# Kernel tuning notes

Measured on AMD Instinct MI355X. Metric: run time of the kernel, lower is better.

## Reference

```python
import jax, jax.numpy as jnp
import numpy as np

N_NODES = 50000
N_EDGES = 800000
IN_DIM, HID_DIM, OUT_DIM = 512, 64, 40
DROPOUT_P = 0.5


def _gcn_conv(h, src, dst, deg_inv_sqrt, W, b, n_nodes):
    # PyG GCNConv (normalize=True, add_self_loops=True):
    #   h' = h @ W; out[dst] += d^-1/2[src] * d^-1/2[dst] * h'[src]; out += b
    # src/dst already include self-loops; deg_inv_sqrt precomputed from them.
    ht = h @ W                                            # [N, F_out]
    norm = deg_inv_sqrt[src] * deg_inv_sqrt[dst]          # [E+N]
    msg = ht[src] * norm[:, None]                         # [E+N, F_out]
    out = jax.ops.segment_sum(msg, dst, num_segments=n_nodes)
    return out + b


def setup_inputs() -> dict:
    key = jax.random.key(0)
    k1, k2, k3, k4 = jax.random.split(key, 4)
    x = jax.random.normal(k1, (N_NODES, IN_DIM), dtype=jnp.float32)
    edge_index = jax.random.randint(k2, (2, N_EDGES), 0, N_NODES, dtype=jnp.int32)
    W1 = jax.random.normal(k3, (IN_DIM, HID_DIM), dtype=jnp.float32) / np.sqrt(IN_DIM)
    b1 = jnp.zeros((HID_DIM,), dtype=jnp.float32)
    W2 = jax.random.normal(k4, (HID_DIM, OUT_DIM), dtype=jnp.float32) / np.sqrt(HID_DIM)
    b2 = jnp.zeros((OUT_DIM,), dtype=jnp.float32)
    return {"x": x, "edge_index": edge_index, "W1": W1, "b1": b1, "W2": W2, "b2": b2}


def reference(x, edge_index, W1, b1, W2, b2):
    n = x.shape[0]
    loop = jnp.arange(n, dtype=edge_index.dtype)
    src = jnp.concatenate([edge_index[0], loop])          # add self-loops
    dst = jnp.concatenate([edge_index[1], loop])
    deg = jax.ops.segment_sum(jnp.ones_like(dst, dtype=x.dtype), dst, num_segments=n)
    deg_inv_sqrt = jnp.where(deg > 0, jax.lax.rsqrt(deg), 0.0)

    h = _gcn_conv(x, src, dst, deg_inv_sqrt, W1, b1, n)
    h = jax.nn.relu(h)
    # dropout (training=True) with a fixed key for determinism
    keep = jax.random.bernoulli(jax.random.key(42), 1.0 - DROPOUT_P, h.shape)
    h = jnp.where(keep, h / (1.0 - DROPOUT_P), 0.0)
    h = _gcn_conv(h, src, dst, deg_inv_sqrt, W2, b2, n)
    return jax.nn.log_softmax(h, axis=1)
```

## Files before the change

kernel.cpp:

```cpp
#include <hip/hip_runtime.h>
#include <math.h>
#include <float.h>

#define N_NODES 50000
#define N_EDGES 800000
#define IN_DIM  512
#define HID_DIM 64
#define OUT_DIM 40
#define GEMM1_BLOCKS 782
#define FILL_BLOCKS 1568
#define NODES_PER_GRP 6250
#define BCAP 96
#define AGG_Q 1563
#define AGG_BLOCKS (8 * AGG_Q)

typedef __attribute__((ext_vector_type(8))) short bf16x8;
typedef __attribute__((ext_vector_type(4))) float f32x4;

__device__ __forceinline__ unsigned rotl32(unsigned v, int n) {
  return (v << n) | (v >> (32 - n));
}

__device__ __forceinline__ void threefry2x32_0_42(unsigned x0, unsigned x1,
                                                  unsigned &o0, unsigned &o1) {
  const unsigned ks0 = 0u;
  const unsigned ks1 = 42u;
  const unsigned ks2 = 0u ^ 42u ^ 0x1BD11BDAu;
  x0 += ks0; x1 += ks1;
  x0 += x1; x1 = rotl32(x1, 13); x1 ^= x0;
  x0 += x1; x1 = rotl32(x1, 15); x1 ^= x0;
  x0 += x1; x1 = rotl32(x1, 26); x1 ^= x0;
  x0 += x1; x1 = rotl32(x1,  6); x1 ^= x0;
  x0 += ks1; x1 += ks2 + 1u;
  x0 += x1; x1 = rotl32(x1, 17); x1 ^= x0;
  x0 += x1; x1 = rotl32(x1, 29); x1 ^= x0;
  x0 += x1; x1 = rotl32(x1, 16); x1 ^= x0;
  x0 += x1; x1 = rotl32(x1, 24); x1 ^= x0;
  x0 += ks2; x1 += ks0 + 2u;
  x0 += x1; x1 = rotl32(x1, 13); x1 ^= x0;
  x0 += x1; x1 = rotl32(x1, 15); x1 ^= x0;
  x0 += x1; x1 = rotl32(x1, 26); x1 ^= x0;
  x0 += x1; x1 = rotl32(x1,  6); x1 ^= x0;
  x0 += ks0; x1 += ks1 + 3u;
  x0 += x1; x1 = rotl32(x1, 17); x1 ^= x0;
  x0 += x1; x1 = rotl32(x1, 29); x1 ^= x0;
  x0 += x1; x1 = rotl32(x1, 16); x1 ^= x0;
  x0 += x1; x1 = rotl32(x1, 24); x1 ^= x0;
  x0 += ks1; x1 += ks2 + 4u;
  x0 += x1; x1 = rotl32(x1, 13); x1 ^= x0;
  x0 += x1; x1 = rotl32(x1, 15); x1 ^= x0;
  x0 += x1; x1 = rotl32(x1, 26); x1 ^= x0;
  x0 += x1; x1 = rotl32(x1,  6); x1 ^= x0;
  x0 += ks2; x1 += ks0 + 5u;
  o0 = x0; o1 = x1;
}

__device__ __forceinline__ unsigned short f2bf(float f) {
  unsigned u = __float_as_uint(f);
  unsigned r = u + 0x7FFFu + ((u >> 16) & 1u);
  return (unsigned short)(r >> 16);
}

__global__ void k_init(const float* __restrict__ W1, const float* __restrict__ W2,
                       unsigned short* __restrict__ Wb1, float* __restrict__ w2t,
                       int* __restrict__ cnt) {
  int i = blockIdx.x * 256 + threadIdx.x;
  if (i < N_NODES) cnt[i] = 0;
  if (i < IN_DIM * HID_DIM) {
    int j = i & 7;
    int lane = (i >> 3) & 63;
    int cg = (i >> 9) & 3;
    int kb = i >> 11;
    int k = kb * 32 + ((lane >> 4) << 3) + j;
    int c = cg * 16 + (lane & 15);
    Wb1[i] = f2bf(W1[k * HID_DIM + c]);
  }
  if (i < HID_DIM * OUT_DIM) {
    int j = i >> 6;
    int k = i & 63;
    w2t[i] = W2[k * OUT_DIM + j];
  }
}

#define XS 136
__global__ __launch_bounds__(512) void k_gemm1_fill(
    const int* __restrict__ ei, int* __restrict__ cnt,
    unsigned short* __restrict__ elist2,
    const float* __restrict__ x, const unsigned short* __restrict__ Wb1,
    unsigned short* __restrict__ ht1b) {
  __shared__ unsigned short sxa[2][64 * XS];

  if (blockIdx.x >= GEMM1_BLOCKS) {
    const int fb = blockIdx.x - GEMM1_BLOCKS;
    const int grp = blockIdx.x & 7;
    const int ord = fb >> 3;
    const int lo = grp * NODES_PER_GRP;
    const int hi = lo + NODES_PER_GRP;
    const int ebase = ord * 512 + threadIdx.x;
    int dv[8];
#pragma unroll
    for (int i = 0; i < 8; ++i) {
      int e = ebase + i * (196 * 512);
      dv[i] = (e < N_EDGES) ? ei[N_EDGES + e] : -1;
    }
#pragma unroll
    for (int i = 0; i < 8; ++i) {
      if (dv[i] >= lo && dv[i] < hi) {
        int s = ei[ebase + i * (196 * 512)];
        int slot = atomicAdd(&cnt[dv[i]], 1);
        if (slot < BCAP) elist2[dv[i] * BCAP + slot] = (unsigned short)s;
      }
    }
    return;
  }

  const int tid = threadIdx.x;
  const int lane = tid & 63;
  const int wave = tid >> 6;
  const int brow = blockIdx.x * 64;
  const int sr = tid >> 3;
  const int sq = tid & 7;

  f32x4 acc[2];
  acc[0] = (f32x4){0.f, 0.f, 0.f, 0.f};
  acc[1] = (f32x4){0.f, 0.f, 0.f, 0.f};

  const bf16x8* __restrict__ Wv = (const bf16x8*)Wb1;
  int gr = brow + sr;
  if (gr >= N_NODES) gr = N_NODES - 1;
  const float* __restrict__ xrow = x + (size_t)gr * IN_DIM;

  float4 lv[4];
#define LOADR(K0)                                                             \
  {                                                                           \
    _Pragma("unroll")                                                         \
    for (int j = 0; j < 4; ++j)                                               \
      lv[j] = *(const float4*)(xrow + (K0) + (sq + j * 8) * 4);               \
  }
#define WRITE(B)                                                              \
  {                                                                           \
    _Pragma("unroll")                                                         \
    for (int j = 0; j < 4; ++j) {                                             \
      ushort4 o;                                                              \
      o.x = f2bf(lv[j].x); o.y = f2bf(lv[j].y);                               \
      o.z = f2bf(lv[j].z); o.w = f2bf(lv[j].w);                               \
      *(ushort4*)(&sxa[B][sr * XS + (sq + j * 8) * 4]) = o;                   \
    }                                                                         \
  }

  LOADR(0)
  WRITE(0)
  __syncthreads();

  const int arow = (16 * (wave & 3) + (lane & 15)) * XS + ((lane >> 4) << 3);
  const int cgb = 2 * (wave >> 2);

  int buf = 0;
  for (int kc = 0; kc < 4; ++kc) {
    if (kc < 3) LOADR((kc + 1) * 128)
#pragma unroll
    for (int ks = 0; ks < 4; ++ks) {
      bf16x8 a = *(const bf16x8*)(&sxa[buf][arow + ks * 32]);
      int kb = kc * 4 + ks;
#pragma unroll
      for (int c = 0; c < 2; ++c) {
        bf16x8 b = Wv[(kb * 4 + cgb + c) * 64 + lane];
        acc[c] = __builtin_amdgcn_mfma_f32_16x16x32_bf16(a, b, acc[c], 0, 0, 0);
      }
    }
    if (kc < 3) WRITE(buf ^ 1)
    __syncthreads();
    buf ^= 1;
  }
#undef LOADR
#undef WRITE

#pragma unroll
  for (int q = 0; q < 4; ++q) {
    int grow = brow + 16 * (wave & 3) + ((lane >> 4) << 2) + q;
    if (grow < N_NODES) {
#pragma unroll
      for (int c = 0; c < 2; ++c) {
        ht1b[(size_t)grow * HID_DIM + (cgb + c) * 16 + (lane & 15)] =
            f2bf(acc[c][q]);
      }
    }
  }
}

__global__ __launch_bounds__(256) void k_agg1g2(const int* __restrict__ cnt,
                                                const unsigned short* __restrict__ elist2,
                                                const unsigned short* __restrict__ ht1b,
                                                const float* __restrict__ b1,
                                                const float* __restrict__ w2t,
                                                unsigned short* __restrict__ ht2b) {
  const int wave = threadIdx.x >> 6;
  const int lane = threadIdx.x & 63;
  const int dl = (blockIdx.x >> 3) * 4 + wave;
  if (dl >= NODES_PER_GRP) return;
  const int d = (blockIdx.x & 7) * NODES_PER_GRP + dl;
  const int g = lane >> 3;
  const int fh = lane & 7;

  unsigned t0, t1;
  threefry2x32_0_42(0u, (unsigned)d * 64u + (unsigned)lane, t0, t1);
  unsigned long long keep = __ballot(!((t0 ^ t1) & 0x80000000u));

  int cn = cnt[d];
  if (cn > BCAP) cn = BCAP;
  const unsigned short* __restrict__ bucket = elist2 + d * BCAP;
  float4 a0 = {0.f, 0.f, 0.f, 0.f};
  float4 a1 = {0.f, 0.f, 0.f, 0.f};
#pragma unroll 2
  for (int j = g; j < cn; j += 8) {
    int s = bucket[j];
    float ds = rsqrtf((float)cnt[s] + 1.0f);
    const uint2* __restrict__ p = (const uint2*)(ht1b + (size_t)s * HID_DIM);
    uint2 q0 = p[fh];
    uint2 q1 = p[fh + 8];
    a0.x += __uint_as_float(q0.x << 16) * ds;
    a0.y += __uint_as_float(q0.x & 0xFFFF0000u) * ds;
    a0.z += __uint_as_float(q0.y << 16) * ds;
    a0.w += __uint_as_float(q0.y & 0xFFFF0000u) * ds;
    a1.x += __uint_as_float(q1.x << 16) * ds;
    a1.y += __uint_as_float(q1.x & 0xFFFF0000u) * ds;
    a1.z += __uint_as_float(q1.y << 16) * ds;
    a1.w += __uint_as_float(q1.y & 0xFFFF0000u) * ds;
  }
#pragma unroll
  for (int m = 32; m >= 8; m >>= 1) {
    a0.x += __shfl_xor(a0.x, m); a0.y += __shfl_xor(a0.y, m);
    a0.z += __shfl_xor(a0.z, m); a0.w += __shfl_xor(a0.w, m);
    a1.x += __shfl_xor(a1.x, m); a1.y += __shfl_xor(a1.y, m);
    a1.z += __shfl_xor(a1.z, m); a1.w += __shfl_xor(a1.w, m);
  }

  float dd = rsqrtf((float)cn + 1.0f);
  {
    const uint2* __restrict__ ps = (const uint2*)(ht1b + (size_t)d * HID_DIM);
    uint2 s0 = ps[fh];
    uint2 s1 = ps[fh + 8];
    a0.x += __uint_as_float(s0.x << 16) * dd;
    a0.y += __uint_as_float(s0.x & 0xFFFF0000u) * dd;
    a0.z += __uint_as_float(s0.y << 16) * dd;
    a0.w += __uint_as_float(s0.y & 0xFFFF0000u) * dd;
    a1.x += __uint_as_float(s1.x << 16) * dd;
    a1.y += __uint_as_float(s1.x & 0xFFFF0000u) * dd;
    a1.z += __uint_as_float(s1.y << 16) * dd;
    a1.w += __uint_as_float(s1.y & 0xFFFF0000u) * dd;
  }
  float4 bb0 = *(const float4*)(b1 + fh * 4);
  float4 bb1 = *(const float4*)(b1 + fh * 4 + 32);
  int f0 = fh * 4;
  float4 v0, v1;
  v0.x = fmaxf(a0.x * dd + bb0.x, 0.f) * (((keep >> (f0 + 0)) & 1) ? 2.f : 0.f);
  v0.y = fmaxf(a0.y * dd + bb0.y, 0.f) * (((keep >> (f0 + 1)) & 1) ? 2.f : 0.f);
  v0.z = fmaxf(a0.z * dd + bb0.z, 0.f) * (((keep >> (f0 + 2)) & 1) ? 2.f : 0.f);
  v0.w = fmaxf(a0.w * dd + bb0.w, 0.f) * (((keep >> (f0 + 3)) & 1) ? 2.f : 0.f);
  v1.x = fmaxf(a1.x * dd + bb1.x, 0.f) * (((keep >> (f0 + 32)) & 1) ? 2.f : 0.f);
  v1.y = fmaxf(a1.y * dd + bb1.y, 0.f) * (((keep >> (f0 + 33)) & 1) ? 2.f : 0.f);
  v1.z = fmaxf(a1.z * dd + bb1.z, 0.f) * (((keep >> (f0 + 34)) & 1) ? 2.f : 0.f);
  v1.w = fmaxf(a1.w * dd + bb1.w, 0.f) * (((keep >> (f0 + 35)) & 1) ? 2.f : 0.f);

  const int jb = g * 5;
  float part[5];
#pragma unroll
  for (int c = 0; c < 5; ++c) {
    const float* __restrict__ wr = w2t + (jb + c) * 64;
    float4 wA = *(const float4*)(wr + f0);
    float4 wB = *(const float4*)(wr + 32 + f0);
    part[c] = v0.x * wA.x + v0.y * wA.y + v0.z * wA.z + v0.w * wA.w +
              v1.x * wB.x + v1.y * wB.y + v1.z * wB.z + v1.w * wB.w;
  }
#pragma unroll
  for (int c = 0; c < 5; ++c) {
    part[c] += __shfl_xor(part[c], 1);
    part[c] += __shfl_xor(part[c], 2);
    part[c] += __shfl_xor(part[c], 4);
  }
  if (fh == 0) {
#pragma unroll
    for (int c = 0; c < 5; ++c)
      ht2b[(size_t)d * OUT_DIM + jb + c] = f2bf(part[c] * dd);
  }
}

__global__ __launch_bounds__(256) void k_agg2(const int* __restrict__ cnt,
                                              const unsigned short* __restrict__ elist2,
                                              const unsigned short* __restrict__ ht2b,
                                              const float* __restrict__ b2,
                                              float* __restrict__ out) {
  const int wave = threadIdx.x >> 6;
  const int lane = threadIdx.x & 63;
  const int dl = (blockIdx.x >> 3) * 4 + wave;
  if (dl >= NODES_PER_GRP) return;
  const int d = (blockIdx.x & 7) * NODES_PER_GRP + dl;
  const int g = lane >> 3;
  const int fh = lane & 7;
  const bool extra = fh < 2;

  int cn = cnt[d];
  if (cn > BCAP) cn = BCAP;
  const unsigned short* __restrict__ bucket = elist2 + d * BCAP;
  float4 a0 = {0.f, 0.f, 0.f, 0.f};
  float4 a1 = {0.f, 0.f, 0.f, 0.f};
#pragma unroll 2
  for (int j = g; j < cn; j += 8) {
    int s = bucket[j];
    const uint2* __restrict__ p = (const uint2*)(ht2b + (size_t)s * OUT_DIM);
    uint2 q0 = p[fh];
    a0.x += __uint_as_float(q0.x << 16);
    a0.y += __uint_as_float(q0.x & 0xFFFF0000u);
    a0.z += __uint_as_float(q0.y << 16);
    a0.w += __uint_as_float(q0.y & 0xFFFF0000u);
    if (extra) {
      uint2 q1 = p[8 + fh];
      a1.x += __uint_as_float(q1.x << 16);
      a1.y += __uint_as_float(q1.x & 0xFFFF0000u);
      a1.z += __uint_as_float(q1.y << 16);
      a1.w += __uint_as_float(q1.y & 0xFFFF0000u);
    }
  }
#pragma unroll
  for (int m = 32; m >= 8; m >>= 1) {
    a0.x += __shfl_xor(a0.x, m); a0.y += __shfl_xor(a0.y, m);
    a0.z += __shfl_xor(a0.z, m); a0.w += __shfl_xor(a0.w, m);
    a1.x += __shfl_xor(a1.x, m); a1.y += __shfl_xor(a1.y, m);
    a1.z += __shfl_xor(a1.z, m); a1.w += __shfl_xor(a1.w, m);
  }

  {
    const uint2* __restrict__ ps = (const uint2*)(ht2b + (size_t)d * OUT_DIM);
    uint2 s0 = ps[fh];
    a0.x += __uint_as_float(s0.x << 16);
    a0.y += __uint_as_float(s0.x & 0xFFFF0000u);
    a0.z += __uint_as_float(s0.y << 16);
    a0.w += __uint_as_float(s0.y & 0xFFFF0000u);
    if (extra) {
      uint2 s1 = ps[8 + fh];
      a1.x += __uint_as_float(s1.x << 16);
      a1.y += __uint_as_float(s1.x & 0xFFFF0000u);
      a1.z += __uint_as_float(s1.y << 16);
      a1.w += __uint_as_float(s1.y & 0xFFFF0000u);
    }
  }

  float dd = rsqrtf((float)cn + 1.0f);
  float4 bb0 = *(const float4*)(b2 + fh * 4);
  float4 v0, v1;
  v0.x = a0.x * dd + bb0.x;
  v0.y = a0.y * dd + bb0.y;
  v0.z = a0.z * dd + bb0.z;
  v0.w = a0.w * dd + bb0.w;
  float mm = fmaxf(fmaxf(v0.x, v0.y), fmaxf(v0.z, v0.w));
  if (extra) {
    float4 bb1 = *(const float4*)(b2 + 32 + fh * 4);
    v1.x = a1.x * dd + bb1.x;
    v1.y = a1.y * dd + bb1.y;
    v1.z = a1.z * dd + bb1.z;
    v1.w = a1.w * dd + bb1.w;
    mm = fmaxf(mm, fmaxf(fmaxf(v1.x, v1.y), fmaxf(v1.z, v1.w)));
  }
  mm = fmaxf(mm, __shfl_xor(mm, 1));
  mm = fmaxf(mm, __shfl_xor(mm, 2));
  mm = fmaxf(mm, __shfl_xor(mm, 4));
  float e = expf(v0.x - mm) + expf(v0.y - mm) + expf(v0.z - mm) + expf(v0.w - mm);
  if (extra)
    e += expf(v1.x - mm) + expf(v1.y - mm) + expf(v1.z - mm) + expf(v1.w - mm);
  e += __shfl_xor(e, 1);
  e += __shfl_xor(e, 2);
  e += __shfl_xor(e, 4);
  float ls = logf(e) + mm;

  if (g == 0) {
    float4 r;
    r.x = v0.x - ls; r.y = v0.y - ls; r.z = v0.z - ls; r.w = v0.w - ls;
    *(float4*)(out + (size_t)d * OUT_DIM + fh * 4) = r;
    if (extra) {
      float4 r1;
      r1.x = v1.x - ls; r1.y = v1.y - ls; r1.z = v1.z - ls; r1.w = v1.w - ls;
      *(float4*)(out + (size_t)d * OUT_DIM + 32 + fh * 4) = r1;
    }
  }
}

extern "C" void kernel_launch(void* const* d_in, const int* in_sizes, int n_in,
                              void* d_out, int out_size, void* d_ws, size_t ws_size,
                              hipStream_t stream) {
  const float* x  = (const float*)d_in[0];
  const int*   ei = (const int*)  d_in[1];
  const float* W1 = (const float*)d_in[2];
  const float* b1 = (const float*)d_in[3];
  const float* W2 = (const float*)d_in[4];
  const float* b2 = (const float*)d_in[5];
  float* out = (float*)d_out;
  float* ws  = (float*)d_ws;

  unsigned short* ht1b = (unsigned short*)ws;
  unsigned short* ht2b = (unsigned short*)(ws + 1600000);
  unsigned short* Wb1 = (unsigned short*)(ws + 2600000);
  float* w2t  = ws + 2620000;
  int* cnt    = (int*)(ws + 2630000);
  unsigned short* elist2 = (unsigned short*)(ws + 2681200);

  k_init<<<196, 256, 0, stream>>>(W1, W2, Wb1, w2t, cnt);
  k_gemm1_fill<<<GEMM1_BLOCKS + FILL_BLOCKS, 512, 0, stream>>>(ei, cnt, elist2,
                                                               x, Wb1, ht1b);
  k_agg1g2<<<AGG_BLOCKS, 256, 0, stream>>>(cnt, elist2, ht1b, b1, w2t, ht2b);
  k_agg2<<<AGG_BLOCKS, 256, 0, stream>>>(cnt, elist2, ht2b, b2, out);
}
```

Baseline: 131.9 us.

## Stream fp32 x tiles into LDS via global_load_lds with XOR swizzle

New measurement: 129.7 us. About the same (-1.6%).

```diff
diff --git a/kernel.cpp b/kernel.cpp
--- a/kernel.cpp
+++ b/kernel.cpp
@@ -16,6 +16,11 @@
 
 typedef __attribute__((ext_vector_type(8))) short bf16x8;
 typedef __attribute__((ext_vector_type(4))) float f32x4;
+
+#define GLOAD_LDS(SRC, DST)                                                   \
+  __builtin_amdgcn_global_load_lds(                                           \
+      (const __attribute__((address_space(1))) void*)(SRC),                   \
+      (__attribute__((address_space(3))) void*)(DST), 16, 0, 0)
 
 __device__ __forceinline__ unsigned rotl32(unsigned v, int n) {
   return (v << n) | (v >> (32 - n));
@@ -82,13 +87,12 @@
   }
 }
 
-#define XS 136
 __global__ __launch_bounds__(512) void k_gemm1_fill(
     const int* __restrict__ ei, int* __restrict__ cnt,
     unsigned short* __restrict__ elist2,
     const float* __restrict__ x, const unsigned short* __restrict__ Wb1,
     unsigned short* __restrict__ ht1b) {
-  __shared__ unsigned short sxa[2][64 * XS];
+  __shared__ unsigned char sxa[2][16384];
 
   if (blockIdx.x >= GEMM1_BLOCKS) {
     const int fb = blockIdx.x - GEMM1_BLOCKS;
@@ -118,62 +122,67 @@
   const int lane = tid & 63;
   const int wave = tid >> 6;
   const int brow = blockIdx.x * 64;
-  const int sr = tid >> 3;
-  const int sq = tid & 7;
 
   f32x4 acc[2];
   acc[0] = (f32x4){0.f, 0.f, 0.f, 0.f};
   acc[1] = (f32x4){0.f, 0.f, 0.f, 0.f};
 
   const bf16x8* __restrict__ Wv = (const bf16x8*)Wb1;
-  int gr = brow + sr;
-  if (gr >= N_NODES) gr = N_NODES - 1;
-  const float* __restrict__ xrow = x + (size_t)gr * IN_DIM;
-
-  float4 lv[4];
-#define LOADR(K0)                                                             \
+
+  int srow[2], soff[2];
+#pragma unroll
+  for (int i = 0; i < 2; ++i) {
+    int p = wave * 2048 + i * 1024 + lane * 16;
+    int row = p >> 8;
+    int b = p & 255;
+    int gr2 = brow + row;
+    if (gr2 >= N_NODES) gr2 = N_NODES - 1;
+    srow[i] = gr2;
+    soff[i] = b ^ ((row & 7) << 4);
+  }
+
+#define ISSUE(B, KC)                                                          \
   {                                                                           \
     _Pragma("unroll")                                                         \
-    for (int j = 0; j < 4; ++j)                                               \
-      lv[j] = *(const float4*)(xrow + (K0) + (sq + j * 8) * 4);               \
-  }
-#define WRITE(B)                                                              \
-  {                                                                           \
-    _Pragma("unroll")                                                         \
-    for (int j = 0; j < 4; ++j) {                                             \
-      ushort4 o;                                                              \
-      o.x = f2bf(lv[j].x); o.y = f2bf(lv[j].y);                               \
-      o.z = f2bf(lv[j].z); o.w = f2bf(lv[j].w);                               \
-      *(ushort4*)(&sxa[B][sr * XS + (sq + j * 8) * 4]) = o;                   \
+    for (int i = 0; i < 2; ++i) {                                             \
+      const char* src = (const char*)(x + (size_t)srow[i] * IN_DIM +          \
+                                      (KC) * 64) + soff[i];                   \
+      GLOAD_LDS(src, &sxa[B][wave * 2048 + i * 1024]);                        \
     }                                                                         \
   }
 
-  LOADR(0)
-  WRITE(0)
+  ISSUE(0, 0)
   __syncthreads();
 
-  const int arow = (16 * (wave & 3) + (lane & 15)) * XS + ((lane >> 4) << 3);
+  const int arow = 16 * (wave & 3) + (lane & 15);
+  const int rsw = (arow & 7) << 4;
+  const int kbyte = (lane >> 4) << 5;
   const int cgb = 2 * (wave >> 2);
 
   int buf = 0;
-  for (int kc = 0; kc < 4; ++kc) {
-    if (kc < 3) LOADR((kc + 1) * 128)
-#pragma unroll
-    for (int ks = 0; ks < 4; ++ks) {
-      bf16x8 a = *(const bf16x8*)(&sxa[buf][arow + ks * 32]);
-      int kb = kc * 4 + ks;
+  for (int kc = 0; kc < 8; ++kc) {
+    if (kc < 7) ISSUE(buf ^ 1, kc + 1)
+#pragma unroll
+    for (int ks = 0; ks < 2; ++ks) {
+      int lin = arow * 256 + ks * 128 + kbyte;
+      float4 fa = *(const float4*)(&sxa[buf][lin ^ rsw]);
+      float4 fb = *(const float4*)(&sxa[buf][(lin + 16) ^ rsw]);
+      union { unsigned short u[8]; bf16x8 v; } pk;
+      pk.u[0] = f2bf(fa.x); pk.u[1] = f2bf(fa.y);
+      pk.u[2] = f2bf(fa.z); pk.u[3] = f2bf(fa.w);
+      pk.u[4] = f2bf(fb.x); pk.u[5] = f2bf(fb.y);
+      pk.u[6] = f2bf(fb.z); pk.u[7] = f2bf(fb.w);
+      int kb = kc * 2 + ks;
 #pragma unroll
       for (int c = 0; c < 2; ++c) {
         bf16x8 b = Wv[(kb * 4 + cgb + c) * 64 + lane];
-        acc[c] = __builtin_amdgcn_mfma_f32_16x16x32_bf16(a, b, acc[c], 0, 0, 0);
+        acc[c] = __builtin_amdgcn_mfma_f32_16x16x32_bf16(pk.v, b, acc[c], 0, 0, 0);
       }
     }
-    if (kc < 3) WRITE(buf ^ 1)
     __syncthreads();
     buf ^= 1;
   }
-#undef LOADR
-#undef WRITE
+#undef ISSUE
 
 #pragma unroll
   for (int q = 0; q < 4; ++q) {
```
